# Optimization experiments

Measured on AMD Instinct MI355X. Metric: run time of the kernel, lower is better.

The kernel has to match this reference:

```python
import jax, jax.numpy as jnp
import numpy as np

H = 32          # hidden_size
NUM_LAYERS = 3
B, T, IN = 16384, 64, 2


def _gru_dir(x, Wih, Whh, bih, bhh, reverse):
    """Single-direction GRU over x:[B,T,I] with PyTorch gate math."""
    # Precompute input projections for all timesteps: [B,T,3H]
    xg = jnp.einsum('bti,gi->btg', x, Wih) + bih
    if reverse:
        xg = xg[:, ::-1]

    def step(h, xt):
        gh = h @ Whh.T + bhh                      # [B,3H]
        xr, xz, xn = jnp.split(xt, 3, axis=-1)
        hr, hz, hn = jnp.split(gh, 3, axis=-1)
        r = jax.nn.sigmoid(xr + hr)
        z = jax.nn.sigmoid(xz + hz)
        n = jnp.tanh(xn + r * hn)
        h2 = (1.0 - z) * n + z * h
        return h2, h2

    h0 = jnp.zeros((x.shape[0], H), x.dtype)
    _, hs = jax.lax.scan(step, h0, jnp.swapaxes(xg, 0, 1))  # [T,B,H]
    hs = jnp.swapaxes(hs, 0, 1)                              # [B,T,H]
    if reverse:
        hs = hs[:, ::-1]
    return hs


def setup_inputs() -> dict:
    key = jax.random.key(0)
    ks = jax.random.split(key, 11)
    s = 0.2  # weight scale ~ uniform(-1/sqrt(H)) magnitude
    return {
        'x':    jax.random.normal(ks[0], (B, T, IN), jnp.float32),
        'Wih0': jax.random.normal(ks[1], (2, 3 * H, IN), jnp.float32) * s,
        'Whh0': jax.random.normal(ks[2], (2, 3 * H, H), jnp.float32) * s,
        'bih0': jax.random.normal(ks[3], (2, 3 * H), jnp.float32) * s,
        'bhh0': jax.random.normal(ks[4], (2, 3 * H), jnp.float32) * s,
        'Wih':  jax.random.normal(ks[5], (NUM_LAYERS - 1, 2, 3 * H, 2 * H), jnp.float32) * s,
        'Whh':  jax.random.normal(ks[6], (NUM_LAYERS - 1, 2, 3 * H, H), jnp.float32) * s,
        'bih':  jax.random.normal(ks[7], (NUM_LAYERS - 1, 2, 3 * H), jnp.float32) * s,
        'bhh':  jax.random.normal(ks[8], (NUM_LAYERS - 1, 2, 3 * H), jnp.float32) * s,
        'Wfc':  jax.random.normal(ks[9], (2, 2 * H), jnp.float32) * s,
        'bfc':  jax.random.normal(ks[10], (2,), jnp.float32) * s,
    }


def reference(x, Wih0, Whh0, bih0, bhh0, Wih, Whh, bih, bhh, Wfc, bfc):
    out = x
    for l in range(NUM_LAYERS):
        if l == 0:
            wi, wh, bi, bh = Wih0, Whh0, bih0, bhh0
        else:
            wi, wh, bi, bh = Wih[l - 1], Whh[l - 1], bih[l - 1], bhh[l - 1]
        fwd = _gru_dir(out, wi[0], wh[0], bi[0], bh[0], reverse=False)
        bwd = _gru_dir(out, wi[1], wh[1], bi[1], bh[1], reverse=True)
        out = jnp.concatenate([fwd, bwd], axis=-1)  # [B,T,2H]
    y = out @ Wfc.T + bfc                            # [B,T,2]
    return jnp.tanh(y)
```

## Files before the change

### kernel.cpp

```cpp
#include <hip/hip_runtime.h>
#include <cstdint>
#include <cstddef>


#define BB 16384
#define TT 64
#define ST ((size_t)BB * 64)

typedef __attribute__((ext_vector_type(8))) _Float16 f16x8;
typedef __attribute__((ext_vector_type(4))) float f32x4;

#if __has_builtin(__builtin_amdgcn_exp2f)
#define EXP2(x) __builtin_amdgcn_exp2f(x)
#else
#define EXP2(x) exp2f(x)
#endif
#if __has_builtin(__builtin_amdgcn_rcpf)
#define RCP(x) __builtin_amdgcn_rcpf(x)
#else
#define RCP(x) (1.0f / (x))
#endif

#define SR (-1.4426950408889634f)
#define SN (-2.8853900817779268f)

__device__ __forceinline__ float tanh_fast(float x) { return 2.0f / (1.0f + __expf(-2.0f * x)) - 1.0f; }
__device__ __forceinline__ unsigned short f2h(float f) {
    _Float16 h = (_Float16)f;
    return __builtin_bit_cast(unsigned short, h);
}
__device__ __forceinline__ unsigned int cvt_pkh(float a, float b) {
#if __has_builtin(__builtin_amdgcn_cvt_pkrtz)
    typedef __fp16 h2_t __attribute__((ext_vector_type(2)));
    h2_t p = __builtin_amdgcn_cvt_pkrtz(a, b);
    return __builtin_bit_cast(unsigned int, p);
#else
    return (unsigned int)f2h(a) | ((unsigned int)f2h(b) << 16);
#endif
}
__device__ __forceinline__ f32x4 mfma16h(f16x8 a, f16x8 b, f32x4 c) {
    return __builtin_amdgcn_mfma_f32_16x16x32_f16(a, b, c, 0, 0, 0);
}

__device__ __forceinline__ void gate_pair(float aR0, float aR1, float aZ0, float aZ1,
                                          float xN0, float xN1, float hN0, float hN1,
                                          float& hp0, float& hp1) {
    float er0 = EXP2(aR0), er1 = EXP2(aR1);
    float ez0 = EXP2(aZ0), ez1 = EXP2(aZ1);
    float Ar0 = 1.f + er0, Ar1 = 1.f + er1;
    float Az0 = 1.f + ez0, Az1 = 1.f + ez1;
    float iR = RCP(Ar0 * Ar1);
    float iZ = RCP(Az0 * Az1);
    float r0 = iR * Ar1, r1 = iR * Ar0;
    float z0 = iZ * Az1, z1 = iZ * Az0;
    float v0 = fmaf(r0, hN0, xN0), v1 = fmaf(r1, hN1, xN1);
    float en0 = EXP2(v0), en1 = EXP2(v1);
    float An0 = 1.f + en0, An1 = 1.f + en1;
    float iN = RCP(An0 * An1);
    float n0 = fmaf(2.f, iN * An1, -1.f);
    float n1 = fmaf(2.f, iN * An0, -1.f);
    hp0 = fmaf(z0, hp0 - n0, n0);
    hp1 = fmaf(z1, hp1 - n1, n1);
}


template<bool IS_L0>
__global__ __launch_bounds__(256, 2)
void gru_mfma(const float* __restrict__ x0,
              const unsigned short* __restrict__ bin,
              const float* __restrict__ Wih,
              const float* __restrict__ Whh,
              const float* __restrict__ bih,
              const float* __restrict__ bhh,
              unsigned short* __restrict__ bout)
{
    const int tid  = threadIdx.x;
    const int lane = tid & 63;
    const int wv   = tid >> 6;
    const int g    = blockIdx.x * 4 + wv;
    const int d    = g >> 10;
    const int b0   = (g & 1023) * 16;
    const int col  = lane & 15;
    const int qd   = lane >> 4;

    f16x8 whhF[6];
    {
        const float* wsrc = Whh + d * 96 * 32;
        #pragma unroll
        for (int t = 0; t < 6; ++t) {
            const float sc = (t < 4) ? SR : SN;
            const int row = (t >> 1) * 32 + 8 * (col >> 2) + 4 * (t & 1) + (col & 3);
            const float* pr = wsrc + row * 32 + qd * 8;
            unsigned short wbits[8];
            #pragma unroll
            for (int j = 0; j < 8; ++j) wbits[j] = f2h(pr[j] * sc);
            whhF[t] = __builtin_bit_cast(f16x8, *(uint4*)wbits);
        }
    }

    f16x8 wihF[6][2];
    float w0c[6][4], w1c[6][4];
    if constexpr (!IS_L0) {
        const float* wsrc = Wih + d * 96 * 64;
        #pragma unroll
        for (int t = 0; t < 6; ++t) {
            const float sc = (t < 4) ? SR : SN;
            const int row = (t >> 1) * 32 + 8 * (col >> 2) + 4 * (t & 1) + (col & 3);
            #pragma unroll
            for (int kc = 0; kc < 2; ++kc) {
                const float* pr = wsrc + row * 64 + kc * 32 + qd * 8;
                unsigned short wbits[8];
                #pragma unroll
                for (int j = 0; j < 8; ++j) wbits[j] = f2h(pr[j] * sc);
                wihF[t][kc] = __builtin_bit_cast(f16x8, *(uint4*)wbits);
            }
        }
    } else {
        #pragma unroll
        for (int t = 0; t < 6; ++t) {
            const float sc = (t < 4) ? SR : SN;
            #pragma unroll
            for (int q = 0; q < 4; ++q) {
                const int row = (t >> 1) * 32 + 8 * qd + 4 * (t & 1) + q;
                const float* pr = Wih + d * 96 * 2 + row * 2;
                w0c[t][q] = pr[0] * sc;
                w1c[t][q] = pr[1] * sc;
            }
        }
    }

    f32x4 biasIn[6], biasHN[2];
    {
        const float* bi = bih + d * 96;
        const float* bh = bhh + d * 96;
        #pragma unroll
        for (int t = 0; t < 4; ++t) {
            const int off = (t >> 1) * 32 + 8 * qd + 4 * (t & 1);
            float4 a = *(const float4*)(bi + off);
            float4 b = *(const float4*)(bh + off);
            biasIn[t][0] = (a.x + b.x) * SR; biasIn[t][1] = (a.y + b.y) * SR;
            biasIn[t][2] = (a.z + b.z) * SR; biasIn[t][3] = (a.w + b.w) * SR;
        }
        #pragma unroll
        for (int T = 0; T < 2; ++T) {
            const int off = 64 + 8 * qd + 4 * T;
            float4 a = *(const float4*)(bi + off);
            float4 b = *(const float4*)(bh + off);
            biasIn[4 + T][0] = a.x * SN; biasIn[4 + T][1] = a.y * SN;
            biasIn[4 + T][2] = a.z * SN; biasIn[4 + T][3] = a.w * SN;
            biasHN[T][0] = b.x * SN; biasHN[T][1] = b.y * SN;
            biasHN[T][2] = b.z * SN; biasHN[T][3] = b.w * SN;
        }
    }

    const int t0 = d ? (TT - 1) : 0;
    const int dt = d ? -1 : 1;
    const ptrdiff_t dplane = (ptrdiff_t)dt * (ptrdiff_t)ST;

    f16x8 hF = {};
    float hprev[2][4] = {{0.f,0.f,0.f,0.f},{0.f,0.f,0.f,0.f}};

    auto REC = [&](f32x4 (&acc)[6], f32x4 (&accHN)[2]) {
        #pragma unroll
        for (int t = 0; t < 4; ++t)
            acc[t] = mfma16h(whhF[t], hF, acc[t]);
        #pragma unroll
        for (int T = 0; T < 2; ++T)
            accHN[T] = mfma16h(whhF[4 + T], hF, biasHN[T]);
    };

    auto PROJ = [&](f32x4 (&accN)[6], uint4 nx0, uint4 nx1, float2 nxs) {
        if constexpr (!IS_L0) {
            f16x8 a0 = __builtin_bit_cast(f16x8, nx0);
            f16x8 a1 = __builtin_bit_cast(f16x8, nx1);
            #pragma unroll
            for (int t = 0; t < 6; ++t) {
                accN[t] = mfma16h(wihF[t][0], a0, biasIn[t]);
                accN[t] = mfma16h(wihF[t][1], a1, accN[t]);
            }
        } else {
            #pragma unroll
            for (int t = 0; t < 6; ++t)
                #pragma unroll
                for (int q = 0; q < 4; ++q)
                    accN[t][q] = fmaf(nxs.x, w0c[t][q], fmaf(nxs.y, w1c[t][q], biasIn[t][q]));
        }
    };

    auto GATES = [&](f32x4 (&acc)[6], f32x4 (&accHN)[2], unsigned short* outp,
                     uint4& hwP, unsigned short*& opP) {
        unsigned int hw[4];
        #pragma unroll
        for (int T = 0; T < 2; ++T) {
            float h0 = hprev[T][0], h1 = hprev[T][1];
            float h2 = hprev[T][2], h3 = hprev[T][3];
            gate_pair(acc[T][0], acc[T][1], acc[2 + T][0], acc[2 + T][1],
                      acc[4 + T][0], acc[4 + T][1], accHN[T][0], accHN[T][1], h0, h1);
            gate_pair(acc[T][2], acc[T][3], acc[2 + T][2], acc[2 + T][3],
                      acc[4 + T][2], acc[4 + T][3], accHN[T][2], accHN[T][3], h2, h3);
            hprev[T][0] = h0; hprev[T][1] = h1; hprev[T][2] = h2; hprev[T][3] = h3;
            hw[2 * T]     = cvt_pkh(h0, h1);
            hw[2 * T + 1] = cvt_pkh(h2, h3);
        }
        hF = __builtin_bit_cast(f16x8, *(uint4*)hw);
        *(uint4*)opP = hwP;
        hwP = *(uint4*)hw;
        opP = outp;
    };

    f32x4 accA[6], accB[6], accHN[2];
    uint4 xc0 = {}, xc1 = {}, xe0 = {}, xe1 = {};
    float2 xsc = {}, xse = {};
    const unsigned short* xptrE = nullptr; const unsigned short* xptrO = nullptr;
    const float* xfpE = nullptr; const float* xfpO = nullptr;

    if constexpr (!IS_L0) {
        const unsigned short* p0 = bin + (size_t)t0 * ST + (size_t)(b0 + col) * 64 + qd * 8;
        uint4 a = *(const uint4*)p0, b = *(const uint4*)(p0 + 32);
        PROJ(accA, a, b, {});
        const unsigned short* p1 = p0 + dplane;
        xc0 = *(const uint4*)p1; xc1 = *(const uint4*)(p1 + 32);
        xptrE = p0 + 2 * dplane;
        xptrO = p0 + 3 * dplane;
    } else {
        const float* p0 = x0 + ((size_t)(b0 + col) * TT + t0) * 2;
        float2 xs0 = *(const float2*)p0;
        PROJ(accA, {}, {}, xs0);
        xsc = *(const float2*)(p0 + dt * 2);
        xfpE = p0 + dt * 4;
        xfpO = p0 + dt * 6;
    }
    unsigned short* optrA = bout + (size_t)t0 * ST + (size_t)(b0 + col) * 64 + d * 32 + qd * 8;
    unsigned short* optrB = optrA + dplane;

    uint4 hwPrevA = {}, hwPrevB = {};
    unsigned short* opPrevA = optrA;
    unsigned short* opPrevB = optrB;

    for (int k = 0; k < 31; ++k) {
        if constexpr (!IS_L0) {
            xe0 = *(const uint4*)xptrE; xe1 = *(const uint4*)(xptrE + 32);
            xptrE += 2 * dplane;
        } else { xse = *(const float2*)xfpE; xfpE += dt * 4; }
        REC(accA, accHN);
        PROJ(accB, xc0, xc1, xsc);
        GATES(accA, accHN, optrA, hwPrevA, opPrevA); optrA += 2 * dplane;
        if constexpr (!IS_L0) {
            xc0 = *(const uint4*)xptrO; xc1 = *(const uint4*)(xptrO + 32);
            xptrO += 2 * dplane;
        } else { xsc = *(const float2*)xfpO; xfpO += dt * 4; }
        REC(accB, accHN);
        PROJ(accA, xe0, xe1, xse);
        GATES(accB, accHN, optrB, hwPrevB, opPrevB); optrB += 2 * dplane;
    }
    REC(accA, accHN);
    PROJ(accB, xc0, xc1, xsc);
    GATES(accA, accHN, optrA, hwPrevA, opPrevA);
    REC(accB, accHN);
    GATES(accB, accHN, optrB, hwPrevB, opPrevB);
    *(uint4*)opPrevA = hwPrevA;
    *(uint4*)opPrevB = hwPrevB;
}

__global__ __launch_bounds__(256)
void fc_kernel(const unsigned short* __restrict__ bin,
               const float* __restrict__ Wfc,
               const float* __restrict__ bfc,
               float* __restrict__ out)
{
    __shared__ float sw[128];
    __shared__ float sb[2];
    const int tid = threadIdx.x;
    if (tid < 128) sw[tid] = Wfc[tid];
    if (tid < 2) sb[tid] = bfc[tid];
    __syncthreads();

    const size_t uidx = (size_t)blockIdx.x * 256 + tid;
    const size_t t = uidx >> 14;
    const size_t b = uidx & (BB - 1);
    const unsigned short* ip = bin + uidx * 64;
    float a0 = sb[0], a1 = sb[1];
    #pragma unroll
    for (int i = 0; i < 64; i += 8) {
        uint4 raw = *(const uint4*)(ip + i);
        #pragma unroll
        for (int w = 0; w < 4; ++w) {
            unsigned int uu = ((const unsigned int*)&raw)[w];
            float f0 = (float)__builtin_bit_cast(_Float16, (unsigned short)(uu & 0xffffu));
            float f1 = (float)__builtin_bit_cast(_Float16, (unsigned short)(uu >> 16));
            a0 = fmaf(f0, sw[i + 2 * w], a0);
            a1 = fmaf(f0, sw[64 + i + 2 * w], a1);
            a0 = fmaf(f1, sw[i + 2 * w + 1], a0);
            a1 = fmaf(f1, sw[64 + i + 2 * w + 1], a1);
        }
    }
    float2 o;
    o.x = tanh_fast(a0);
    o.y = tanh_fast(a1);
    *(float2*)&out[(b * TT + t) * 2] = o;
}

extern "C" void kernel_launch(void* const* d_in, const int* in_sizes, int n_in,
                              void* d_out, int out_size, void* d_ws, size_t ws_size,
                              hipStream_t stream)
{
    const float* x    = (const float*)d_in[0];
    const float* Wih0 = (const float*)d_in[1];
    const float* Whh0 = (const float*)d_in[2];
    const float* bih0 = (const float*)d_in[3];
    const float* bhh0 = (const float*)d_in[4];
    const float* WihL = (const float*)d_in[5];
    const float* WhhL = (const float*)d_in[6];
    const float* bihL = (const float*)d_in[7];
    const float* bhhL = (const float*)d_in[8];
    const float* Wfc  = (const float*)d_in[9];
    const float* bfc  = (const float*)d_in[10];

    unsigned short* buf0 = (unsigned short*)d_ws;
    unsigned short* buf1 = buf0 + (size_t)TT * BB * 64;
    float* out = (float*)d_out;

    gru_mfma<true><<<512, 256, 0, stream>>>(
        x, nullptr, Wih0, Whh0, bih0, bhh0, buf0);
    gru_mfma<false><<<512, 256, 0, stream>>>(
        nullptr, buf0, WihL, WhhL, bihL, bhhL, buf1);
    gru_mfma<false><<<512, 256, 0, stream>>>(
        nullptr, buf1, WihL + 2 * 96 * 64, WhhL + 2 * 96 * 32,
        bihL + 2 * 96, bhhL + 2 * 96, buf0);
    fc_kernel<<<(BB * TT) / 256, 256, 0, stream>>>(buf0, Wfc, bfc, out);
}
```

Measured before the change: 316.8 us.

## Fuse final FC projection into last GRU layer, emit per-direction partial sums

```diff
diff --git a/kernel.cpp b/kernel.cpp
--- a/kernel.cpp
+++ b/kernel.cpp
@@ -6,6 +6,7 @@
 #define BB 16384
 #define TT 64
 #define ST ((size_t)BB * 64)
+#define PT ((size_t)TT * BB * 2)
 
 typedef __attribute__((ext_vector_type(8))) _Float16 f16x8;
 typedef __attribute__((ext_vector_type(4))) float f32x4;
@@ -64,7 +65,7 @@
 }
 
 
-template<bool IS_L0>
+template<bool IS_L0, bool IS_LAST>
 __global__ __launch_bounds__(256, 2)
 void gru_mfma(const float* __restrict__ x0,
               const unsigned short* __restrict__ bin,
@@ -72,7 +73,9 @@
               const float* __restrict__ Whh,
               const float* __restrict__ bih,
               const float* __restrict__ bhh,
-              unsigned short* __restrict__ bout)
+              unsigned short* __restrict__ bout,
+              const float* __restrict__ Wfc,
+              float* __restrict__ pbase)
 {
     const int tid  = threadIdx.x;
     const int lane = tid & 63;
@@ -153,6 +156,18 @@
         }
     }
 
+    float wf0[2][4], wf1[2][4];
+    if constexpr (IS_LAST) {
+        #pragma unroll
+        for (int T = 0; T < 2; ++T)
+            #pragma unroll
+            for (int q = 0; q < 4; ++q) {
+                const int u = 8 * qd + 4 * T + q;
+                wf0[T][q] = Wfc[d * 32 + u];
+                wf1[T][q] = Wfc[64 + d * 32 + u];
+            }
+    }
+
     const int t0 = d ? (TT - 1) : 0;
     const int dt = d ? -1 : 1;
     const ptrdiff_t dplane = (ptrdiff_t)dt * (ptrdiff_t)ST;
@@ -188,7 +203,7 @@
     };
 
     auto GATES = [&](f32x4 (&acc)[6], f32x4 (&accHN)[2], unsigned short* outp,
-                     uint4& hwP, unsigned short*& opP) {
+                     uint4& hwP, unsigned short*& opP, float* poutp) {
         unsigned int hw[4];
         #pragma unroll
         for (int T = 0; T < 2; ++T) {
@@ -203,9 +218,23 @@
             hw[2 * T + 1] = cvt_pkh(h2, h3);
         }
         hF = __builtin_bit_cast(f16x8, *(uint4*)hw);
-        *(uint4*)opP = hwP;
-        hwP = *(uint4*)hw;
-        opP = outp;
+        if constexpr (IS_LAST) {
+            float p0 = 0.f, p1 = 0.f;
+            #pragma unroll
+            for (int T = 0; T < 2; ++T)
+                #pragma unroll
+                for (int q = 0; q < 4; ++q) {
+                    p0 = fmaf(hprev[T][q], wf0[T][q], p0);
+                    p1 = fmaf(hprev[T][q], wf1[T][q], p1);
+                }
+            p0 += __shfl_xor(p0, 16); p0 += __shfl_xor(p0, 32);
+            p1 += __shfl_xor(p1, 16); p1 += __shfl_xor(p1, 32);
+            if (qd == 0) *(float2*)poutp = make_float2(p0, p1);
+        } else {
+            *(uint4*)opP = hwP;
+            hwP = *(uint4*)hw;
+            opP = outp;
+        }
     };
 
     f32x4 accA[6], accB[6], accHN[2];
@@ -230,8 +259,17 @@
         xfpE = p0 + dt * 4;
         xfpO = p0 + dt * 6;
     }
-    unsigned short* optrA = bout + (size_t)t0 * ST + (size_t)(b0 + col) * 64 + d * 32 + qd * 8;
-    unsigned short* optrB = optrA + dplane;
+
+    unsigned short* optrA = nullptr; unsigned short* optrB = nullptr;
+    float* poutA = nullptr; float* poutB = nullptr;
+    const ptrdiff_t dpp = (ptrdiff_t)dt * (ptrdiff_t)BB * 2;
+    if constexpr (IS_LAST) {
+        poutA = pbase + (size_t)d * PT + ((size_t)t0 * BB + b0 + col) * 2;
+        poutB = poutA + dpp;
+    } else {
+        optrA = bout + (size_t)t0 * ST + (size_t)(b0 + col) * 64 + d * 32 + qd * 8;
+        optrB = optrA + dplane;
+    }
 
     uint4 hwPrevA = {}, hwPrevB = {};
     unsigned short* opPrevA = optrA;
@@ -244,60 +282,57 @@
         } else { xse = *(const float2*)xfpE; xfpE += dt * 4; }
         REC(accA, accHN);
         PROJ(accB, xc0, xc1, xsc);
-        GATES(accA, accHN, optrA, hwPrevA, opPrevA); optrA += 2 * dplane;
+        GATES(accA, accHN, optrA, hwPrevA, opPrevA, poutA);
+        if constexpr (IS_LAST) poutA += 2 * dpp; else optrA += 2 * dplane;
         if constexpr (!IS_L0) {
             xc0 = *(const uint4*)xptrO; xc1 = *(const uint4*)(xptrO + 32);
             xptrO += 2 * dplane;
         } else { xsc = *(const float2*)xfpO; xfpO += dt * 4; }
         REC(accB, accHN);
         PROJ(accA, xe0, xe1, xse);
-        GATES(accB, accHN, optrB, hwPrevB, opPrevB); optrB += 2 * dplane;
+        GATES(accB, accHN, optrB, hwPrevB, opPrevB, poutB);
+        if constexpr (IS_LAST) poutB += 2 * dpp; else optrB += 2 * dplane;
     }
     REC(accA, accHN);
     PROJ(accB, xc0, xc1, xsc);
-    GATES(accA, accHN, optrA, hwPrevA, opPrevA);
+    GATES(accA, accHN, optrA, hwPrevA, opPrevA, poutA);
     REC(accB, accHN);
-    GATES(accB, accHN, optrB, hwPrevB, opPrevB);
-    *(uint4*)opPrevA = hwPrevA;
-    *(uint4*)opPrevB = hwPrevB;
+    GATES(accB, accHN, optrB, hwPrevB, opPrevB, poutB);
+    if constexpr (!IS_LAST) {
+        *(uint4*)opPrevA = hwPrevA;
+        *(uint4*)opPrevB = hwPrevB;
+    }
 }
 
 __global__ __launch_bounds__(256)
-void fc_kernel(const unsigned short* __restrict__ bin,
-               const float* __restrict__ Wfc,
+void fc_finish(const float* __restrict__ pf,
+               const float* __restrict__ pb,
                const float* __restrict__ bfc,
                float* __restrict__ out)
 {
-    __shared__ float sw[128];
-    __shared__ float sb[2];
+    __shared__ float2 tile[64][65];
     const int tid = threadIdx.x;
-    if (tid < 128) sw[tid] = Wfc[tid];
-    if (tid < 2) sb[tid] = bfc[tid];
+    const int bbase = blockIdx.x * 64;
+    const float c0 = bfc[0], c1 = bfc[1];
+    #pragma unroll
+    for (int tp = 0; tp < 16; ++tp) {
+        const int t = tp * 4 + (tid >> 6);
+        const int bl = tid & 63;
+        const size_t idx = ((size_t)t * BB + bbase + bl) * 2;
+        float2 vf = *(const float2*)(pf + idx);
+        float2 vb = *(const float2*)(pb + idx);
+        float2 o;
+        o.x = tanh_fast(vf.x + vb.x + c0);
+        o.y = tanh_fast(vf.y + vb.y + c1);
+        tile[t][bl] = o;
+    }
     __syncthreads();
-
-    const size_t uidx = (size_t)blockIdx.x * 256 + tid;
-    const size_t t = uidx >> 14;
-    const size_t b = uidx & (BB - 1);
-    const unsigned short* ip = bin + uidx * 64;
-    float a0 = sb[0], a1 = sb[1];
     #pragma unroll
-    for (int i = 0; i < 64; i += 8) {
-        uint4 raw = *(const uint4*)(ip + i);
-        #pragma unroll
-        for (int w = 0; w < 4; ++w) {
-            unsigned int uu = ((const unsigned int*)&raw)[w];
-            float f0 = (float)__builtin_bit_cast(_Float16, (unsigned short)(uu & 0xffffu));
-            float f1 = (float)__builtin_bit_cast(_Float16, (unsigned short)(uu >> 16));
-            a0 = fmaf(f0, sw[i + 2 * w], a0);
-            a1 = fmaf(f0, sw[64 + i + 2 * w], a1);
-            a0 = fmaf(f1, sw[i + 2 * w + 1], a0);
-            a1 = fmaf(f1, sw[64 + i + 2 * w + 1], a1);
-        }
-    }
-    float2 o;
-    o.x = tanh_fast(a0);
-    o.y = tanh_fast(a1);
-    *(float2*)&out[(b * TT + t) * 2] = o;
+    for (int bp = 0; bp < 16; ++bp) {
+        const int bl = bp * 4 + (tid >> 6);
+        const int t = tid & 63;
+        *(float2*)(out + ((size_t)(bbase + bl) * TT + t) * 2) = tile[t][bl];
+    }
 }
 
 extern "C" void kernel_launch(void* const* d_in, const int* in_sizes, int n_in,
@@ -318,14 +353,16 @@
 
     unsigned short* buf0 = (unsigned short*)d_ws;
     unsigned short* buf1 = buf0 + (size_t)TT * BB * 64;
+    float* pbase = (float*)d_ws;
     float* out = (float*)d_out;
 
-    gru_mfma<true><<<512, 256, 0, stream>>>(
-        x, nullptr, Wih0, Whh0, bih0, bhh0, buf0);
-    gru_mfma<false><<<512, 256, 0, stream>>>(
-        nullptr, buf0, WihL, WhhL, bihL, bhhL, buf1);
-    gru_mfma<false><<<512, 256, 0, stream>>>(
+    gru_mfma<true, false><<<512, 256, 0, stream>>>(
+        x, nullptr, Wih0, Whh0, bih0, bhh0, buf0, nullptr, nullptr);
+    gru_mfma<false, false><<<512, 256, 0, stream>>>(
+        nullptr, buf0, WihL, WhhL, bihL, bhhL, buf1, nullptr, nullptr);
+    gru_mfma<false, true><<<512, 256, 0, stream>>>(
         nullptr, buf1, WihL + 2 * 96 * 64, WhhL + 2 * 96 * 32,
-        bihL + 2 * 96, bhhL + 2 * 96, buf0);
-    fc_kernel<<<(BB * TT) / 256, 256, 0, stream>>>(buf0, Wfc, bfc, out);
-}
+        bihL + 2 * 96, bhhL + 2 * 96, nullptr, Wfc, pbase);
+    fc_finish<<<BB / 64, 256, 0, stream>>>(
+        pbase, pbase + PT, bfc, out);
+}
```

New measurement: 304.3 us. -3.9%, faster.
